# Optimization experiments

Hardware: AMD Instinct MI355X
Metric: run time of the kernel (lower is better)

The kernel has to match this reference:

```python
import jax, jax.numpy as jnp
import numpy as np

HEAD_NUM = 16
EMB_DIM = 1024
PROJ_DIM = 1024
CONTEXT_LEN = 2048
HEAD_DIM = PROJ_DIM // HEAD_NUM


def setup_inputs() -> dict:
    key = jax.random.key(0)
    k_x, k_q, k_k, k_v, k_o = jax.random.split(key, 5)
    scale = 0.02
    X_emb = jax.random.normal(k_x, (2, CONTEXT_LEN, EMB_DIM), dtype=jnp.float32)
    W_q = jax.random.normal(k_q, (EMB_DIM, PROJ_DIM), dtype=jnp.float32) * scale
    W_k = jax.random.normal(k_k, (EMB_DIM, PROJ_DIM), dtype=jnp.float32) * scale
    W_v = jax.random.normal(k_v, (EMB_DIM, PROJ_DIM), dtype=jnp.float32) * scale
    W_out = jax.random.normal(k_o, (PROJ_DIM, PROJ_DIM), dtype=jnp.float32) * scale
    return {"X_emb": X_emb, "W_q": W_q, "W_k": W_k, "W_v": W_v, "W_out": W_out}


def reference(X_emb, W_q, W_k, W_v, W_out):
    B, S, _ = X_emb.shape
    H, D = HEAD_NUM, HEAD_DIM
    # QKV projections (no bias), split into heads: [B, H, S, D]
    q = (X_emb @ W_q).reshape(B, S, H, D).transpose(0, 2, 1, 3)
    k = (X_emb @ W_k).reshape(B, S, H, D).transpose(0, 2, 1, 3)
    v = (X_emb @ W_v).reshape(B, S, H, D).transpose(0, 2, 1, 3)
    # Raw scores [B, H, S, S]; causal mask applied BEFORE scaling (as in source;
    # -inf is invariant under the subsequent division so math matches).
    scores = jnp.einsum("bhqd,bhkd->bhqk", q, k)
    causal = jnp.triu(jnp.ones((S, S), dtype=bool), k=1)  # True above diagonal
    scores = jnp.where(causal, -jnp.inf, scores)
    scores = scores / jnp.asarray(np.sqrt(D), dtype=scores.dtype)
    att_w = jax.nn.softmax(scores, axis=-1)
    # dropout_rate = 0.0 -> identity
    ctx = jnp.einsum("bhqk,bhkd->bhqd", att_w, v)
    ctx = ctx.transpose(0, 2, 1, 3).reshape(B, S, H * D)
    return ctx @ W_out
```

## Files before the change

### kernel.cpp

```cpp
#include <hip/hip_runtime.h>
#include <stdint.h>

#define SEQ   2048
#define EMB   1024
#define PROJ  1024
#define HEADS 16
#define HD    64
#define BATCH 2
#define MROWS (BATCH * SEQ)
#define QKVN  3072

typedef __attribute__((ext_vector_type(8))) __bf16 bf16x8;
typedef __attribute__((ext_vector_type(4))) __bf16 bf16x4;
typedef __attribute__((ext_vector_type(4))) float  f32x4;

static __device__ __forceinline__ __bf16 f2b(float f) {
  union { float f; uint32_t u; } a; a.f = f;
  uint32_t r = a.u + 0x7FFFu + ((a.u >> 16) & 1u);
  union { uint16_t u; __bf16 b; } o; o.u = (uint16_t)(r >> 16);
  return o.b;
}

#define GLOAD_LDS16(gsrc, ldst)                                                \
  __builtin_amdgcn_global_load_lds(                                            \
      (const __attribute__((address_space(1))) void*)(gsrc),                   \
      (__attribute__((address_space(3))) void*)(ldst), 16, 0, 0)

__global__ void cast_f32_bf16(const float* __restrict__ in,
                              __bf16* __restrict__ out, int n) {
  int i = (blockIdx.x * blockDim.x + threadIdx.x) * 4;
  if (i + 3 < n) {
    float4 v = *reinterpret_cast<const float4*>(in + i);
    bf16x4 o;
    o[0] = f2b(v.x); o[1] = f2b(v.y); o[2] = f2b(v.z); o[3] = f2b(v.w);
    *reinterpret_cast<bf16x4*>(out + i) = o;
  }
}

__global__ void transpose_cast(const float* __restrict__ W0, const float* __restrict__ W1,
                               const float* __restrict__ W2, const float* __restrict__ W3,
                               __bf16* __restrict__ Tqkv, __bf16* __restrict__ To) {
  const float* W; __bf16* T;
  switch (blockIdx.z) {
    case 0: W = W0; T = Tqkv;                       break;
    case 1: W = W1; T = Tqkv + (size_t)1024 * 1024; break;
    case 2: W = W2; T = Tqkv + (size_t)2048 * 1024; break;
    default: W = W3; T = To;                        break;
  }
  __shared__ float tile[32][33];
  int k0 = blockIdx.x * 32, n0 = blockIdx.y * 32;
  int tx = threadIdx.x & 31, ty = threadIdx.x >> 5;
#pragma unroll
  for (int r = ty; r < 32; r += 8)
    tile[r][tx] = W[(size_t)(k0 + r) * 1024 + n0 + tx];
  __syncthreads();
#pragma unroll
  for (int r = ty; r < 32; r += 8)
    T[(size_t)(n0 + r) * 1024 + k0 + tx] = f2b(tile[tx][r]);
}

template <int BM, bool OUT_BF16, bool SCALE_Q, bool VSPLIT>
__global__ __launch_bounds__(256) void gemm_bt(const __bf16* __restrict__ A,
                                               const __bf16* __restrict__ Bt,
                                               void* __restrict__ Cout,
                                               __bf16* __restrict__ vt,
                                               int M, int N, int K) {
  constexpr int MI = BM / 32;
  __shared__ __align__(16) __bf16 As[BM * 32];
  __shared__ __align__(16) __bf16 Bs[128 * 32];
  const int t = threadIdx.x;
  const int lane = t & 63, w = t >> 6;
  const int g = lane >> 4, l15 = lane & 15;
  const int m0 = blockIdx.x * BM, n0 = blockIdx.y * 128;
  const int wr = w >> 1, wc = w & 1;

  f32x4 acc[MI][4];
#pragma unroll
  for (int i = 0; i < MI; i++)
#pragma unroll
    for (int j = 0; j < 4; j++) acc[i][j] = {0.f, 0.f, 0.f, 0.f};

  for (int k0 = 0; k0 < K; k0 += 32) {
    __syncthreads();
#pragma unroll
    for (int c = t; c < BM * 4; c += 256)
      GLOAD_LDS16(A + (size_t)(m0 + (c >> 2)) * K + k0 + (c & 3) * 8, As + c * 8);
#pragma unroll
    for (int c = t; c < 512; c += 256)
      GLOAD_LDS16(Bt + (size_t)(n0 + (c >> 2)) * K + k0 + (c & 3) * 8, Bs + c * 8);
    __syncthreads();

    bf16x8 af[MI], bfr[4];
#pragma unroll
    for (int mi = 0; mi < MI; mi++)
      af[mi] = *reinterpret_cast<const bf16x8*>(As + (wr * (BM / 2) + mi * 16 + l15) * 32 + g * 8);
#pragma unroll
    for (int ni = 0; ni < 4; ni++)
      bfr[ni] = *reinterpret_cast<const bf16x8*>(Bs + (wc * 64 + ni * 16 + l15) * 32 + g * 8);
#pragma unroll
    for (int mi = 0; mi < MI; mi++)
#pragma unroll
      for (int ni = 0; ni < 4; ni++)
        acc[mi][ni] = __builtin_amdgcn_mfma_f32_16x16x32_bf16(af[mi], bfr[ni], acc[mi][ni], 0, 0, 0);
  }

#pragma unroll
  for (int mi = 0; mi < MI; mi++)
#pragma unroll
    for (int ni = 0; ni < 4; ni++) {
      int row = m0 + wr * (BM / 2) + mi * 16 + g * 4;
      int col = n0 + wc * 64 + ni * 16 + l15;
      if (VSPLIT && col >= 2048) {
        int hd = col - 2048;
        int bb = row >> 11, ss = row & 2047;
        bf16x4 v4;
#pragma unroll
        for (int r = 0; r < 4; r++) v4[r] = f2b(acc[mi][ni][r]);
        *reinterpret_cast<bf16x4*>(vt + ((size_t)((bb * 16 + (hd >> 6)) * 64 + (hd & 63))) * 2048 + ss) = v4;
      } else {
#pragma unroll
        for (int r = 0; r < 4; r++) {
          float v = acc[mi][ni][r];
          if (SCALE_Q && col < 1024) v *= 0.125f;
          if (OUT_BF16)
            ((__bf16*)Cout)[(size_t)(row + r) * N + col] = f2b(v);
          else
            ((float*)Cout)[(size_t)(row + r) * N + col] = v;
        }
      }
    }
}

__global__ __launch_bounds__(256, 2) void attn_fwd(const __bf16* __restrict__ QKV,
                                                   const __bf16* __restrict__ Vt,
                                                   __bf16* __restrict__ ctx) {
  const int id = blockIdx.x;
  const int bh = (id & 7) * 4 + ((id >> 3) & 3);
  const int mi = 31 - (id >> 5);
  const int b = bh >> 4, h = bh & 15;
  const int tid = threadIdx.x, lane = tid & 63, w = tid >> 6;
  const int g = lane >> 4, l15 = lane & 15;

  __shared__ __align__(16) __bf16 Ks[2][64 * 64];
  __shared__ __align__(16) __bf16 Vs[2][64 * 64];
  __shared__ __align__(16) __bf16 P_lds[4][16][72];

  const __bf16* Qg  = QKV + (size_t)b * SEQ * QKVN + h * 64;
  const __bf16* Kg  = Qg + 1024;
  const __bf16* VtH = Vt + (size_t)bh * 64 * 2048;
  __bf16* Cg = ctx + (size_t)b * SEQ * 1024 + h * 64;

  const int r0 = tid >> 3, j0 = tid & 7;
  const int r1 = r0 + 32;
  const int ls0 = r0 * 64 + ((j0 ^ (r0 & 7)) * 8);
  const int ls1 = r1 * 64 + ((j0 ^ (r1 & 7)) * 8);
  const size_t gk0 = (size_t)r0 * QKVN + j0 * 8;
  const size_t gk1 = (size_t)r1 * QKVN + j0 * 8;
  const size_t gv0 = (size_t)r0 * 2048 + j0 * 8;
  const size_t gv1 = (size_t)r1 * 2048 + j0 * 8;
  const int xw = l15 & 7;

  const int qw = mi * 64 + 16 * w;
  const int Tm = mi + 1;

  bf16x8 qf[2];
#pragma unroll
  for (int ks = 0; ks < 2; ks++)
    qf[ks] = *reinterpret_cast<const bf16x8*>(
        Qg + (size_t)(qw + l15) * QKVN + ks * 32 + g * 8);

  f32x4 acco[4];
  float mrun = -1e30f, lrun = 0.f;
#pragma unroll
  for (int nd = 0; nd < 4; nd++) acco[nd] = {0.f, 0.f, 0.f, 0.f};

  {
    bf16x8 ka = *reinterpret_cast<const bf16x8*>(Kg + gk0);
    bf16x8 kb = *reinterpret_cast<const bf16x8*>(Kg + gk1);
    bf16x8 va = *reinterpret_cast<const bf16x8*>(VtH + gv0);
    bf16x8 vc = *reinterpret_cast<const bf16x8*>(VtH + gv1);
    *reinterpret_cast<bf16x8*>(Ks[0] + ls0) = ka;
    *reinterpret_cast<bf16x8*>(Ks[0] + ls1) = kb;
    *reinterpret_cast<bf16x8*>(Vs[0] + ls0) = va;
    *reinterpret_cast<bf16x8*>(Vs[0] + ls1) = vc;
  }
  __syncthreads();

  for (int it = 0; it < Tm; ++it) {
    const int cur = it & 1, nxt = cur ^ 1;
    const bool hn = (it + 1 < Tm);
    bf16x8 ka, kb, va, vc;
    if (hn) {
      const size_t kvn = (size_t)(it + 1) * 64;
      ka = *reinterpret_cast<const bf16x8*>(Kg + kvn * QKVN + gk0);
      kb = *reinterpret_cast<const bf16x8*>(Kg + kvn * QKVN + gk1);
      va = *reinterpret_cast<const bf16x8*>(VtH + kvn + gv0);
      vc = *reinterpret_cast<const bf16x8*>(VtH + kvn + gv1);
    }

    {
      const int kv0 = it * 64;
      const bool diag = (it == Tm - 1);
      const __bf16* Kc = Ks[cur];
      const __bf16* Vc = Vs[cur];

      bf16x8 kf[4][2], vb[4][2];
#pragma unroll
      for (int nb = 0; nb < 4; nb++) {
        const int row = (nb * 16 + l15) * 64;
#pragma unroll
        for (int ks = 0; ks < 2; ks++) {
          const int co = ((ks * 4 + g) ^ xw) * 8;
          kf[nb][ks] = *reinterpret_cast<const bf16x8*>(Kc + row + co);
          vb[nb][ks] = *reinterpret_cast<const bf16x8*>(Vc + row + co);
        }
      }

      f32x4 accS[4];
#pragma unroll
      for (int nb = 0; nb < 4; nb++) accS[nb] = {0.f, 0.f, 0.f, 0.f};
#pragma unroll
      for (int nb = 0; nb < 4; nb++) {
        accS[nb] = __builtin_amdgcn_mfma_f32_16x16x32_bf16(kf[nb][0], qf[0], accS[nb], 0, 0, 0);
        accS[nb] = __builtin_amdgcn_mfma_f32_16x16x32_bf16(kf[nb][1], qf[1], accS[nb], 0, 0, 0);
      }

      if (diag) {
        const int qi = qw + l15;
#pragma unroll
        for (int nb = 0; nb < 4; nb++)
#pragma unroll
          for (int r = 0; r < 4; r++) {
            int kvi = kv0 + nb * 16 + g * 4 + r;
            if (kvi > qi) accS[nb][r] = -1e30f;
          }
      }

      {
        float pmax = -1e30f;
#pragma unroll
        for (int nb = 0; nb < 4; nb++)
#pragma unroll
          for (int r = 0; r < 4; r++) pmax = fmaxf(pmax, accS[nb][r]);
        pmax = fmaxf(pmax, __shfl_xor(pmax, 16));
        pmax = fmaxf(pmax, __shfl_xor(pmax, 32));
        if (!__all(pmax <= mrun + 8.0f)) {
          float mnew = fmaxf(mrun, pmax);
          float corr = __expf(mrun - mnew);
          mrun = mnew;
          lrun *= corr;
#pragma unroll
          for (int r = 0; r < 4; r++) {
            float cr = __shfl(corr, (g << 4) + (g << 2) + r);
#pragma unroll
            for (int nd = 0; nd < 4; nd++) acco[nd][r] *= cr;
          }
        }
        float lsum = 0.f;
#pragma unroll
        for (int nb = 0; nb < 4; nb++) {
          bf16x4 pk;
#pragma unroll
          for (int r = 0; r < 4; r++) {
            float pv = __expf(accS[nb][r] - mrun);
            lsum += pv;
            pk[r] = (__bf16)pv;
          }
          *reinterpret_cast<bf16x4*>(&P_lds[w][l15][nb * 16 + g * 4]) = pk;
        }
        lsum += __shfl_xor(lsum, 16);
        lsum += __shfl_xor(lsum, 32);
        lrun += lsum;
      }

      {
        bf16x8 pa0 = *reinterpret_cast<const bf16x8*>(&P_lds[w][l15][g * 8]);
        bf16x8 pa1 = *reinterpret_cast<const bf16x8*>(&P_lds[w][l15][32 + g * 8]);
#pragma unroll
        for (int nd = 0; nd < 4; nd++) {
          acco[nd] = __builtin_amdgcn_mfma_f32_16x16x32_bf16(pa0, vb[nd][0], acco[nd], 0, 0, 0);
          acco[nd] = __builtin_amdgcn_mfma_f32_16x16x32_bf16(pa1, vb[nd][1], acco[nd], 0, 0, 0);
        }
      }
    }

    if (hn) {
      *reinterpret_cast<bf16x8*>(Ks[nxt] + ls0) = ka;
      *reinterpret_cast<bf16x8*>(Ks[nxt] + ls1) = kb;
      *reinterpret_cast<bf16x8*>(Vs[nxt] + ls0) = va;
      *reinterpret_cast<bf16x8*>(Vs[nxt] + ls1) = vc;
    }
    __syncthreads();
  }

  {
    float inv = 1.0f / lrun;
#pragma unroll
    for (int r = 0; r < 4; r++) {
      float ir = __shfl(inv, (g << 4) + (g << 2) + r);
      int qrow = qw + g * 4 + r;
#pragma unroll
      for (int nd = 0; nd < 4; nd++)
        Cg[(size_t)qrow * 1024 + nd * 16 + l15] = (__bf16)(acco[nd][r] * ir);
    }
  }
}

extern "C" void kernel_launch(void* const* d_in, const int* in_sizes, int n_in,
                              void* d_out, int out_size, void* d_ws, size_t ws_size,
                              hipStream_t stream) {
  const float* X  = (const float*)d_in[0];
  const float* Wq = (const float*)d_in[1];
  const float* Wk = (const float*)d_in[2];
  const float* Wv = (const float*)d_in[3];
  const float* Wo = (const float*)d_in[4];
  float* out = (float*)d_out;

  uint8_t* ws = (uint8_t*)d_ws;
  size_t off = 0;
  const size_t actBytes = (size_t)MROWS * 1024 * 2;
  __bf16* Xb    = (__bf16*)(ws + off); off += actBytes;
  __bf16* WqkvT = (__bf16*)(ws + off); off += (size_t)QKVN * 1024 * 2;
  __bf16* WoT   = (__bf16*)(ws + off); off += (size_t)1024 * 1024 * 2;
  __bf16* QKV   = (__bf16*)(ws + off); off += (size_t)MROWS * QKVN * 2;
  __bf16* Vt    = (__bf16*)(ws + off); off += actBytes;
  __bf16* Cb    = Xb;

  cast_f32_bf16<<<dim3(MROWS * 1024 / 4 / 256), dim3(256), 0, stream>>>(X, Xb, MROWS * 1024);
  transpose_cast<<<dim3(32, 32, 4), dim3(256), 0, stream>>>(Wq, Wk, Wv, Wo, WqkvT, WoT);

  gemm_bt<128, true, true, true><<<dim3(MROWS / 128, QKVN / 128), dim3(256), 0, stream>>>(
      Xb, WqkvT, QKV, Vt, MROWS, QKVN, EMB);

  attn_fwd<<<dim3(1024), dim3(256), 0, stream>>>(QKV, Vt, Cb);

  gemm_bt<128, false, false, false><<<dim3(MROWS / 128, PROJ / 128), dim3(256), 0, stream>>>(
      Cb, WoT, out, nullptr, MROWS, PROJ, PROJ);
}
```

Measured before the change: 113.3 us.

## Stream K via direct global-to-LDS loads, read V from global, retile out-proj

The attention kernel now stages only K tiles in shared memory, using async global_load_lds copies instead of register round-trips. V fragments are loaded straight from global memory into registers each iteration, so the V shared buffer goes away. MFMA sections are wrapped in s_setprio raises. The output-projection GEMM switches to 64-row tiles to launch more blocks. Uncoalesced per-lane V global loads add latency on the critical path, and the oversized K buffer declaration (8448 elements) looks odd.

```diff
diff --git a/kernel.cpp b/kernel.cpp
--- a/kernel.cpp
+++ b/kernel.cpp
@@ -141,8 +141,7 @@
   const int tid = threadIdx.x, lane = tid & 63, w = tid >> 6;
   const int g = lane >> 4, l15 = lane & 15;
 
-  __shared__ __align__(16) __bf16 Ks[2][64 * 64];
-  __shared__ __align__(16) __bf16 Vs[2][64 * 64];
+  __shared__ __align__(16) __bf16 Ks[2][8448];
   __shared__ __align__(16) __bf16 P_lds[4][16][72];
 
   const __bf16* Qg  = QKV + (size_t)b * SEQ * QKVN + h * 64;
@@ -150,14 +149,6 @@
   const __bf16* VtH = Vt + (size_t)bh * 64 * 2048;
   __bf16* Cg = ctx + (size_t)b * SEQ * 1024 + h * 64;
 
-  const int r0 = tid >> 3, j0 = tid & 7;
-  const int r1 = r0 + 32;
-  const int ls0 = r0 * 64 + ((j0 ^ (r0 & 7)) * 8);
-  const int ls1 = r1 * 64 + ((j0 ^ (r1 & 7)) * 8);
-  const size_t gk0 = (size_t)r0 * QKVN + j0 * 8;
-  const size_t gk1 = (size_t)r1 * QKVN + j0 * 8;
-  const size_t gv0 = (size_t)r0 * 2048 + j0 * 8;
-  const size_t gv1 = (size_t)r1 * 2048 + j0 * 8;
   const int xw = l15 & 7;
 
   const int qw = mi * 64 + 16 * w;
@@ -174,122 +165,119 @@
 #pragma unroll
   for (int nd = 0; nd < 4; nd++) acco[nd] = {0.f, 0.f, 0.f, 0.f};
 
-  {
-    bf16x8 ka = *reinterpret_cast<const bf16x8*>(Kg + gk0);
-    bf16x8 kb = *reinterpret_cast<const bf16x8*>(Kg + gk1);
-    bf16x8 va = *reinterpret_cast<const bf16x8*>(VtH + gv0);
-    bf16x8 vc = *reinterpret_cast<const bf16x8*>(VtH + gv1);
-    *reinterpret_cast<bf16x8*>(Ks[0] + ls0) = ka;
-    *reinterpret_cast<bf16x8*>(Ks[0] + ls1) = kb;
-    *reinterpret_cast<bf16x8*>(Vs[0] + ls0) = va;
-    *reinterpret_cast<bf16x8*>(Vs[0] + ls1) = vc;
+#pragma unroll
+  for (int k2 = 0; k2 < 2; k2++) {
+    const int p = tid + 256 * k2;
+    const int rk = p >> 3, jk = (p & 7) ^ (rk & 7);
+    GLOAD_LDS16(Kg + (size_t)rk * QKVN + jk * 8, Ks[0] + p * 8);
   }
   __syncthreads();
 
   for (int it = 0; it < Tm; ++it) {
-    const int cur = it & 1, nxt = cur ^ 1;
-    const bool hn = (it + 1 < Tm);
-    bf16x8 ka, kb, va, vc;
-    if (hn) {
-      const size_t kvn = (size_t)(it + 1) * 64;
-      ka = *reinterpret_cast<const bf16x8*>(Kg + kvn * QKVN + gk0);
-      kb = *reinterpret_cast<const bf16x8*>(Kg + kvn * QKVN + gk1);
-      va = *reinterpret_cast<const bf16x8*>(VtH + kvn + gv0);
-      vc = *reinterpret_cast<const bf16x8*>(VtH + kvn + gv1);
+    const int cur = it & 1;
+
+    if (it + 1 < Tm) {
+      const int koff = (it + 1) * 64;
+#pragma unroll
+      for (int k2 = 0; k2 < 2; k2++) {
+        const int p = tid + 256 * k2;
+        const int rk = p >> 3, jk = (p & 7) ^ (rk & 7);
+        GLOAD_LDS16(Kg + (size_t)(koff + rk) * QKVN + jk * 8, Ks[cur ^ 1] + p * 8);
+      }
+    }
+
+    const int kv0 = it * 64;
+    const bool diag = (it == Tm - 1);
+
+    bf16x8 vb[4][2];
+#pragma unroll
+    for (int nd = 0; nd < 4; nd++)
+#pragma unroll
+      for (int ks = 0; ks < 2; ks++)
+        vb[nd][ks] = *reinterpret_cast<const bf16x8*>(
+            VtH + (size_t)(nd * 16 + l15) * 2048 + kv0 + ks * 32 + g * 8);
+
+    const __bf16* Kc = Ks[cur];
+    bf16x8 kf[4][2];
+#pragma unroll
+    for (int nb = 0; nb < 4; nb++) {
+      const int row = (nb * 16 + l15) * 64;
+#pragma unroll
+      for (int ks = 0; ks < 2; ks++)
+        kf[nb][ks] = *reinterpret_cast<const bf16x8*>(Kc + row + (((ks * 4 + g) ^ xw) * 8));
+    }
+
+    f32x4 accS[4];
+#pragma unroll
+    for (int nb = 0; nb < 4; nb++) accS[nb] = {0.f, 0.f, 0.f, 0.f};
+    __builtin_amdgcn_s_setprio(1);
+#pragma unroll
+    for (int nb = 0; nb < 4; nb++) {
+      accS[nb] = __builtin_amdgcn_mfma_f32_16x16x32_bf16(kf[nb][0], qf[0], accS[nb], 0, 0, 0);
+      accS[nb] = __builtin_amdgcn_mfma_f32_16x16x32_bf16(kf[nb][1], qf[1], accS[nb], 0, 0, 0);
+    }
+    __builtin_amdgcn_s_setprio(0);
+
+    if (diag) {
+      const int qi = qw + l15;
+#pragma unroll
+      for (int nb = 0; nb < 4; nb++)
+#pragma unroll
+        for (int r = 0; r < 4; r++) {
+          int kvi = kv0 + nb * 16 + g * 4 + r;
+          if (kvi > qi) accS[nb][r] = -1e30f;
+        }
     }
 
     {
-      const int kv0 = it * 64;
-      const bool diag = (it == Tm - 1);
-      const __bf16* Kc = Ks[cur];
-      const __bf16* Vc = Vs[cur];
-
-      bf16x8 kf[4][2], vb[4][2];
+      float pmax = -1e30f;
+#pragma unroll
+      for (int nb = 0; nb < 4; nb++)
+#pragma unroll
+        for (int r = 0; r < 4; r++) pmax = fmaxf(pmax, accS[nb][r]);
+      pmax = fmaxf(pmax, __shfl_xor(pmax, 16));
+      pmax = fmaxf(pmax, __shfl_xor(pmax, 32));
+      if (!__all(pmax <= mrun + 8.0f)) {
+        float mnew = fmaxf(mrun, pmax);
+        float corr = __expf(mrun - mnew);
+        mrun = mnew;
+        lrun *= corr;
+#pragma unroll
+        for (int r = 0; r < 4; r++) {
+          float cr = __shfl(corr, (g << 4) + (g << 2) + r);
+#pragma unroll
+          for (int nd = 0; nd < 4; nd++) acco[nd][r] *= cr;
+        }
+      }
+      float lsum = 0.f;
 #pragma unroll
       for (int nb = 0; nb < 4; nb++) {
-        const int row = (nb * 16 + l15) * 64;
-#pragma unroll
-        for (int ks = 0; ks < 2; ks++) {
-          const int co = ((ks * 4 + g) ^ xw) * 8;
-          kf[nb][ks] = *reinterpret_cast<const bf16x8*>(Kc + row + co);
-          vb[nb][ks] = *reinterpret_cast<const bf16x8*>(Vc + row + co);
+        bf16x4 pk;
+#pragma unroll
+        for (int r = 0; r < 4; r++) {
+          float pv = __expf(accS[nb][r] - mrun);
+          lsum += pv;
+          pk[r] = (__bf16)pv;
         }
-      }
-
-      f32x4 accS[4];
-#pragma unroll
-      for (int nb = 0; nb < 4; nb++) accS[nb] = {0.f, 0.f, 0.f, 0.f};
-#pragma unroll
-      for (int nb = 0; nb < 4; nb++) {
-        accS[nb] = __builtin_amdgcn_mfma_f32_16x16x32_bf16(kf[nb][0], qf[0], accS[nb], 0, 0, 0);
-        accS[nb] = __builtin_amdgcn_mfma_f32_16x16x32_bf16(kf[nb][1], qf[1], accS[nb], 0, 0, 0);
-      }
-
-      if (diag) {
-        const int qi = qw + l15;
-#pragma unroll
-        for (int nb = 0; nb < 4; nb++)
-#pragma unroll
-          for (int r = 0; r < 4; r++) {
-            int kvi = kv0 + nb * 16 + g * 4 + r;
-            if (kvi > qi) accS[nb][r] = -1e30f;
-          }
-      }
-
-      {
-        float pmax = -1e30f;
-#pragma unroll
-        for (int nb = 0; nb < 4; nb++)
-#pragma unroll
-          for (int r = 0; r < 4; r++) pmax = fmaxf(pmax, accS[nb][r]);
-        pmax = fmaxf(pmax, __shfl_xor(pmax, 16));
-        pmax = fmaxf(pmax, __shfl_xor(pmax, 32));
-        if (!__all(pmax <= mrun + 8.0f)) {
-          float mnew = fmaxf(mrun, pmax);
-          float corr = __expf(mrun - mnew);
-          mrun = mnew;
-          lrun *= corr;
-#pragma unroll
-          for (int r = 0; r < 4; r++) {
-            float cr = __shfl(corr, (g << 4) + (g << 2) + r);
-#pragma unroll
-            for (int nd = 0; nd < 4; nd++) acco[nd][r] *= cr;
-          }
-        }
-        float lsum = 0.f;
-#pragma unroll
-        for (int nb = 0; nb < 4; nb++) {
-          bf16x4 pk;
-#pragma unroll
-          for (int r = 0; r < 4; r++) {
-            float pv = __expf(accS[nb][r] - mrun);
-            lsum += pv;
-            pk[r] = (__bf16)pv;
-          }
-          *reinterpret_cast<bf16x4*>(&P_lds[w][l15][nb * 16 + g * 4]) = pk;
-        }
-        lsum += __shfl_xor(lsum, 16);
-        lsum += __shfl_xor(lsum, 32);
-        lrun += lsum;
-      }
-
-      {
-        bf16x8 pa0 = *reinterpret_cast<const bf16x8*>(&P_lds[w][l15][g * 8]);
-        bf16x8 pa1 = *reinterpret_cast<const bf16x8*>(&P_lds[w][l15][32 + g * 8]);
-#pragma unroll
-        for (int nd = 0; nd < 4; nd++) {
-          acco[nd] = __builtin_amdgcn_mfma_f32_16x16x32_bf16(pa0, vb[nd][0], acco[nd], 0, 0, 0);
-          acco[nd] = __builtin_amdgcn_mfma_f32_16x16x32_bf16(pa1, vb[nd][1], acco[nd], 0, 0, 0);
-        }
-      }
-    }
-
-    if (hn) {
-      *reinterpret_cast<bf16x8*>(Ks[nxt] + ls0) = ka;
-      *reinterpret_cast<bf16x8*>(Ks[nxt] + ls1) = kb;
-      *reinterpret_cast<bf16x8*>(Vs[nxt] + ls0) = va;
-      *reinterpret_cast<bf16x8*>(Vs[nxt] + ls1) = vc;
-    }
+        *reinterpret_cast<bf16x4*>(&P_lds[w][l15][nb * 16 + g * 4]) = pk;
+      }
+      lsum += __shfl_xor(lsum, 16);
+      lsum += __shfl_xor(lsum, 32);
+      lrun += lsum;
+    }
+
+    {
+      bf16x8 pa0 = *reinterpret_cast<const bf16x8*>(&P_lds[w][l15][g * 8]);
+      bf16x8 pa1 = *reinterpret_cast<const bf16x8*>(&P_lds[w][l15][32 + g * 8]);
+      __builtin_amdgcn_s_setprio(1);
+#pragma unroll
+      for (int nd = 0; nd < 4; nd++) {
+        acco[nd] = __builtin_amdgcn_mfma_f32_16x16x32_bf16(pa0, vb[nd][0], acco[nd], 0, 0, 0);
+        acco[nd] = __builtin_amdgcn_mfma_f32_16x16x32_bf16(pa1, vb[nd][1], acco[nd], 0, 0, 0);
+      }
+      __builtin_amdgcn_s_setprio(0);
+    }
+
     __syncthreads();
   }
 
@@ -334,6 +322,6 @@
 
   attn_fwd<<<dim3(1024), dim3(256), 0, stream>>>(QKV, Vt, Cb);
 
-  gemm_bt<128, false, false, false><<<dim3(MROWS / 128, PROJ / 128), dim3(256), 0, stream>>>(
+  gemm_bt<64, false, false, false><<<dim3(MROWS / 64, PROJ / 128), dim3(256), 0, stream>>>(
       Cb, WoT, out, nullptr, MROWS, PROJ, PROJ);
 }
```

New measurement: 151.0 us. 33.3% more time.
